# Performance work log

Measured on AMD Instinct MI355X. Metric: run time of the kernel, lower is better.

Reference implementation:

```python
import jax, jax.numpy as jnp
import numpy as np

N, C, H, W = 16, 512, 32, 32
OC = C // 8  # shrink = 8


def setup_inputs() -> dict:
    key = jax.random.key(0)
    ks = jax.random.split(key, 8)
    s = lambda fan: 1.0 / np.sqrt(fan)
    return {
        "tensor": jax.random.normal(ks[0], (N, C, H, W), dtype=jnp.float32),
        "key_w": jax.random.normal(ks[1], (OC, C), dtype=jnp.float32) * s(C),
        "key_b": jax.random.normal(ks[2], (OC,), dtype=jnp.float32) * 0.01,
        "query_w": jax.random.normal(ks[3], (OC, C), dtype=jnp.float32) * s(C),
        "query_b": jax.random.normal(ks[4], (OC,), dtype=jnp.float32) * 0.01,
        "value_w": jax.random.normal(ks[5], (C, C), dtype=jnp.float32) * s(C),
        "value_b": jax.random.normal(ks[6], (C,), dtype=jnp.float32) * 0.01,
        "gamma": jax.random.normal(ks[7], (1,), dtype=jnp.float32),
    }


def reference(tensor, key_w, key_b, query_w, query_b, value_w, value_b, gamma):
    n, c, h, w = tensor.shape
    x = tensor.reshape(n, c, h * w)  # [n, c, hw]
    # 1x1 convs are per-position linear maps over channels
    k = jnp.einsum("oc,ncp->nop", key_w, x) + key_b[None, :, None]      # [n, oc, hw]
    q = jnp.einsum("oc,ncp->nop", query_w, x) + query_b[None, :, None]  # [n, oc, hw]
    v = jnp.einsum("oc,ncp->nop", value_w, x) + value_b[None, :, None]  # [n, c, hw]
    # unscaled attention: softmax over keys (last dim)
    scores = jnp.einsum("ncq,nck->nqk", q, k)  # [n, hw, hw]
    attn = jax.nn.softmax(scores, axis=2)
    o = jnp.einsum("nck,nqk->ncq", v, attn).reshape(n, c, h, w)
    return tensor + o * gamma[0]
```

## Files before the change

kernel.cpp:

```cpp
#include <hip/hip_runtime.h>
#include <hip/hip_bf16.h>

typedef __hip_bfloat16 bf16;
typedef __attribute__((ext_vector_type(8))) short bf16x8;
typedef __attribute__((ext_vector_type(4))) float f32x4;

#define NBATCH 16
#define CCH    512
#define PP     1024
#define OCH    64

__device__ __forceinline__ void gload16(const void* g, void* l) {
  __builtin_amdgcn_global_load_lds(
      (const __attribute__((address_space(1))) void*)g,
      (__attribute__((address_space(3))) void*)l, 16, 0, 0);
}
__device__ __forceinline__ float bf2f(bf16 v) { return __bfloat162float(v); }
__device__ __forceinline__ bf16  f2bf(float v) { return __float2bfloat16(v); }

__device__ __forceinline__ void barrier_vm0() {
  asm volatile("s_waitcnt vmcnt(0)" ::: "memory");
  __builtin_amdgcn_s_barrier();
  asm volatile("" ::: "memory");
}
__device__ __forceinline__ void barrier_lgkm0() {
  asm volatile("s_waitcnt lgkmcnt(0)" ::: "memory");
  __builtin_amdgcn_s_barrier();
  asm volatile("" ::: "memory");
}

__global__ __launch_bounds__(256) void prep_transpose_kernel(
    const float* __restrict__ x,
    const float* __restrict__ key_w, const float* __restrict__ key_b,
    const float* __restrict__ query_w, const float* __restrict__ query_b,
    const float* __restrict__ value_w, const float* __restrict__ value_b,
    bf16* __restrict__ xhi, bf16* __restrict__ xlo,
    bf16* __restrict__ wqk_hi, bf16* __restrict__ wqk_lo,
    bf16* __restrict__ wv, float* __restrict__ bias_qk, float* __restrict__ bias_v) {
  __shared__ float tile[64 * 65];
  const int bid = blockIdx.x;
  const int tid = threadIdx.x;
  if (bid < 2048) {
    const int pt = bid & 15, ct = (bid >> 4) & 7, n = bid >> 7;
    const size_t xbase = ((size_t)n * CCH + ct * 64) * PP + pt * 64;
#pragma unroll
    for (int i = 0; i < 4; ++i) {
      const int chunk = i * 256 + tid;
      const int row = chunk >> 4, c4 = chunk & 15;
      const f32x4 v = *(const f32x4*)&x[xbase + (size_t)row * PP + c4 * 4];
#pragma unroll
      for (int m = 0; m < 4; ++m) tile[row * 65 + c4 * 4 + m] = v[m];
    }
    __syncthreads();
    const size_t obase = ((size_t)n * PP + pt * 64) * CCH + ct * 64;
#pragma unroll
    for (int ii = 0; ii < 2; ++ii) {
      const int p = ii * 32 + (tid >> 3);
      const int cu = tid & 7;
      bf16x8 hv, lv;
#pragma unroll
      for (int j = 0; j < 8; ++j) {
        const float f = tile[(cu * 8 + j) * 65 + p];
        const bf16 h = f2bf(f);
        const bf16 lo_ = f2bf(f - bf2f(h));
        short hs, ls;
        __builtin_memcpy(&hs, &h, 2);
        __builtin_memcpy(&ls, &lo_, 2);
        hv[j] = hs;
        lv[j] = ls;
      }
      const size_t oidx = obase + (size_t)p * CCH + cu * 8;
      *(bf16x8*)&xhi[oidx] = hv;
      *(bf16x8*)&xlo[oidx] = lv;
    }
  } else {
    const int t = (bid - 2048) * 256 + tid;
    const int TOT_QK = 128 * 512;
    const int TOT_V  = 512 * 512;
    if (t < TOT_QK) {
      const int m = t >> 9, c = t & 511;
      const float v = (m < 64) ? query_w[m * 512 + c] : key_w[(m - 64) * 512 + c];
      const bf16 hi = f2bf(v);
      wqk_hi[t] = hi;
      wqk_lo[t] = f2bf(v - bf2f(hi));
    } else if (t < TOT_QK + TOT_V) {
      const int u = t - TOT_QK;
      wv[u] = f2bf(value_w[u]);
    } else if (t < TOT_QK + TOT_V + 128) {
      const int m = t - (TOT_QK + TOT_V);
      bias_qk[m] = (m < 64) ? query_b[m] : key_b[m - 64];
    } else if (t < TOT_QK + TOT_V + 128 + 512) {
      const int m = t - (TOT_QK + TOT_V + 128);
      bias_v[m] = value_b[m];
    }
  }
}

__global__ __launch_bounds__(256) void gemm_qkv_kernel(
    const bf16* __restrict__ Whi, const bf16* __restrict__ Wlo,
    const bf16* __restrict__ Wv,
    const bf16* __restrict__ XThi, const bf16* __restrict__ XTlo,
    const float* __restrict__ biasqk, const float* __restrict__ biasv,
    bf16* __restrict__ qhi, bf16* __restrict__ qlo,
    bf16* __restrict__ khi, bf16* __restrict__ klo,
    bf16* __restrict__ Vout) {
  __shared__ __align__(16) bf16 sm[4 * 128 * 64];
  const int tid = threadIdx.x, l = tid & 63, w = tid >> 6;
  const int lrow = l >> 3, lcol = (l & 7) * 8, wr = w >> 1, wc = w & 1;
  const f32x4 z = {0.f, 0.f, 0.f, 0.f};
  f32x4 acc[4][4];
#pragma unroll
  for (int i = 0; i < 4; ++i)
#pragma unroll
    for (int j = 0; j < 4; ++j) acc[i][j] = z;

  if (blockIdx.x < 128) {
    const int id = blockIdx.x;
    const int n0 = (id & 7) * 128, bn = id >> 3;
    const size_t xoff = (size_t)bn * PP * CCH;
    bf16* Ash = sm;
    bf16* Asl = sm + 8192;
    bf16* Bsh = sm + 16384;
    bf16* Bsl = sm + 24576;
    for (int kt = 0; kt < CCH; kt += 64) {
#pragma unroll
      for (int it = 0; it < 4; ++it) {
        const int chunk = w * 4 + it;
        const int ar = chunk * 8 + lrow;
        const int br = n0 + chunk * 8 + lrow;
        gload16(Whi + (size_t)ar * CCH + kt + lcol, &Ash[chunk * 512]);
        gload16(Wlo + (size_t)ar * CCH + kt + lcol, &Asl[chunk * 512]);
        gload16(XThi + xoff + (size_t)br * CCH + kt + lcol, &Bsh[chunk * 512]);
        gload16(XTlo + xoff + (size_t)br * CCH + kt + lcol, &Bsl[chunk * 512]);
      }
      __syncthreads();
#pragma unroll
      for (int kk = 0; kk < 2; ++kk) {
        bf16x8 ah[4], al[4], bh[4], bl[4];
        const int ko = kk * 32 + (l >> 4) * 8;
#pragma unroll
        for (int i = 0; i < 4; ++i) {
          const int r = (wr * 64 + i * 16 + (l & 15)) * 64 + ko;
          ah[i] = *(const bf16x8*)&Ash[r];
          al[i] = *(const bf16x8*)&Asl[r];
        }
#pragma unroll
        for (int j = 0; j < 4; ++j) {
          const int r = (wc * 64 + j * 16 + (l & 15)) * 64 + ko;
          bh[j] = *(const bf16x8*)&Bsh[r];
          bl[j] = *(const bf16x8*)&Bsl[r];
        }
#pragma unroll
        for (int i = 0; i < 4; ++i)
#pragma unroll
          for (int j = 0; j < 4; ++j) {
            acc[i][j] = __builtin_amdgcn_mfma_f32_16x16x32_bf16(ah[i], bh[j], acc[i][j], 0, 0, 0);
            acc[i][j] = __builtin_amdgcn_mfma_f32_16x16x32_bf16(ah[i], bl[j], acc[i][j], 0, 0, 0);
            acc[i][j] = __builtin_amdgcn_mfma_f32_16x16x32_bf16(al[i], bh[j], acc[i][j], 0, 0, 0);
          }
      }
      __syncthreads();
    }
    const size_t qoff = (size_t)bn * PP * OCH;
#pragma unroll
    for (int i = 0; i < 4; ++i)
#pragma unroll
      for (int j = 0; j < 4; ++j)
#pragma unroll
        for (int r = 0; r < 4; ++r) {
          const int m = wr * 64 + i * 16 + (l >> 4) * 4 + r;
          const int p = n0 + wc * 64 + j * 16 + (l & 15);
          const float v = acc[i][j][r] + biasqk[m];
          const bf16 hi = f2bf(v);
          const bf16 lo = f2bf(v - bf2f(hi));
          if (m < 64) {
            qhi[qoff + (size_t)p * OCH + m] = hi;
            qlo[qoff + (size_t)p * OCH + m] = lo;
          } else {
            khi[qoff + (size_t)p * OCH + (m - 64)] = hi;
            klo[qoff + (size_t)p * OCH + (m - 64)] = lo;
          }
        }
  } else {
    const int id = blockIdx.x - 128;
    const int n0 = (id & 7) * 128, m0 = ((id >> 3) & 3) * 128, bn = id >> 5;
    const size_t xoff = (size_t)bn * PP * CCH;
    bf16* As = sm;
    bf16* Bs = sm + 8192;
    for (int kt = 0; kt < CCH; kt += 64) {
#pragma unroll
      for (int it = 0; it < 4; ++it) {
        const int chunk = w * 4 + it;
        gload16(Wv + (size_t)(m0 + chunk * 8 + lrow) * CCH + kt + lcol, &As[chunk * 512]);
        gload16(XThi + xoff + (size_t)(n0 + chunk * 8 + lrow) * CCH + kt + lcol, &Bs[chunk * 512]);
      }
      __syncthreads();
#pragma unroll
      for (int kk = 0; kk < 2; ++kk) {
        bf16x8 a[4], b[4];
        const int ko = kk * 32 + (l >> 4) * 8;
#pragma unroll
        for (int i = 0; i < 4; ++i) a[i] = *(const bf16x8*)&As[(wr * 64 + i * 16 + (l & 15)) * 64 + ko];
#pragma unroll
        for (int j = 0; j < 4; ++j) b[j] = *(const bf16x8*)&Bs[(wc * 64 + j * 16 + (l & 15)) * 64 + ko];
#pragma unroll
        for (int i = 0; i < 4; ++i)
#pragma unroll
          for (int j = 0; j < 4; ++j)
            acc[i][j] = __builtin_amdgcn_mfma_f32_16x16x32_bf16(a[i], b[j], acc[i][j], 0, 0, 0);
      }
      __syncthreads();
    }
#pragma unroll
    for (int i = 0; i < 4; ++i)
#pragma unroll
      for (int j = 0; j < 4; ++j)
#pragma unroll
        for (int r = 0; r < 4; ++r) {
          const int m = m0 + wr * 64 + i * 16 + (l >> 4) * 4 + r;
          const int p = n0 + wc * 64 + j * 16 + (l & 15);
          Vout[(size_t)bn * CCH * PP + (size_t)m * PP + p] = f2bf(acc[i][j][r] + biasv[m]);
        }
  }
}

#define KT 32
#define NT 32

__global__ __launch_bounds__(512, 2) void fused_attn_kernel(
    const bf16* __restrict__ qhi, const bf16* __restrict__ qlo,
    const bf16* __restrict__ khi, const bf16* __restrict__ klo,
    const bf16* __restrict__ vbuf, const float* __restrict__ tensor,
    const float* __restrict__ gamma, float* __restrict__ out) {
  __shared__ __align__(16) char smem[102400];
  __shared__ float red[128];
  __shared__ float fq[64];
  const int tid = threadIdx.x, l = tid & 63, w = tid >> 6;

  const int d = blockIdx.x;
  const int idx = d >> 3;
  const int bn = (d & 7) * 2 + (idx >> 4);
  const int qt0 = (idx & 15) * 64;

  const size_t qkoff = (size_t)bn * PP * OCH;
  const size_t voff  = (size_t)bn * CCH * PP;
  char* Qh = smem;
  char* Ql = smem + 8192;
  char* Pb = smem + 98304;

  {
    const int s = (w << 6) | l;
    const int row = s >> 3, pu = s & 7, lu = pu ^ (row & 7);
    const size_t src = qkoff + (size_t)(qt0 + row) * OCH + lu * 8;
    gload16(qhi + src, Qh + w * 1024);
    gload16(qlo + src, Ql + w * 1024);
  }
  barrier_vm0();

  bf16x8 ah[2], al[2];
  {
    const int qrow = ((w & 3) << 4) + (l & 15);
#pragma unroll
    for (int h = 0; h < 2; ++h) {
      const int lu = (l >> 4) + 4 * h, pu = lu ^ (qrow & 7);
      ah[h] = *(const bf16x8*)(Qh + qrow * 128 + pu * 16);
      al[h] = *(const bf16x8*)(Ql + qrow * 128 + pu * 16);
    }
  }

  auto stage_kv = [&](int t, char* khD, char* klD, char* vD) {
    {
      const int s = ((w & 3) << 6) | l;
      const int row = s >> 3, pu = s & 7, lu = pu ^ (row & 7);
      const bf16* srcp = ((w < 4) ? khi : klo) + qkoff + (size_t)(t * KT + row) * OCH + lu * 8;
      gload16(srcp, ((w < 4) ? khD : klD) + (w & 3) * 1024);
    }
#pragma unroll
    for (int c4 = 0; c4 < 4; ++c4) {
      const int s = (w << 8) + (c4 << 6) + l;
      const int row = s >> 2, pu = s & 3, lu = pu ^ ((row >> 1) & 3);
      const bf16* srcp = vbuf + voff + (size_t)row * PP + t * KT + lu * 8;
      gload16(srcp, vD + ((w << 8) + (c4 << 6)) * 16);
    }
  };

  stage_kv(0, smem + 16384, smem + 24576, smem + 32768);

  f32x4 acc[4][4];
  const f32x4 z = {0.f, 0.f, 0.f, 0.f};
#pragma unroll
  for (int i = 0; i < 4; ++i)
#pragma unroll
    for (int j = 0; j < 4; ++j) acc[i][j] = z;
  float psum[4] = {0.f, 0.f, 0.f, 0.f};
  const int kf = w >> 2;

  for (int t = 0; t < NT; ++t) {
    char* khB = smem + 16384 + ((t & 1) ? 4096 : 0);
    char* klB = smem + 24576 + ((t & 1) ? 4096 : 0);
    char* vB  = smem + 32768 + ((t & 1) ? 32768 : 0);

    barrier_vm0();

    if (t + 1 < NT) {
      stage_kv(t + 1,
               smem + 16384 + ((t & 1) ? 0 : 4096),
               smem + 24576 + ((t & 1) ? 0 : 4096),
               smem + 32768 + ((t & 1) ? 0 : 32768));
    }

    bf16x8 kh_[2], kl_[2];
    const int krow = (kf << 4) + (l & 15);
#pragma unroll
    for (int h = 0; h < 2; ++h) {
      const int lu = (l >> 4) + 4 * h, pu = lu ^ (krow & 7);
      kh_[h] = *(const bf16x8*)(khB + krow * 128 + pu * 16);
      kl_[h] = *(const bf16x8*)(klB + krow * 128 + pu * 16);
    }
    __builtin_amdgcn_s_setprio(1);
    f32x4 s = z;
    s = __builtin_amdgcn_mfma_f32_16x16x32_bf16(ah[0], kh_[0], s, 0, 0, 0);
    s = __builtin_amdgcn_mfma_f32_16x16x32_bf16(ah[1], kh_[1], s, 0, 0, 0);
    s = __builtin_amdgcn_mfma_f32_16x16x32_bf16(al[0], kh_[0], s, 0, 0, 0);
    s = __builtin_amdgcn_mfma_f32_16x16x32_bf16(al[1], kh_[1], s, 0, 0, 0);
    s = __builtin_amdgcn_mfma_f32_16x16x32_bf16(ah[0], kl_[0], s, 0, 0, 0);
    s = __builtin_amdgcn_mfma_f32_16x16x32_bf16(ah[1], kl_[1], s, 0, 0, 0);
    __builtin_amdgcn_s_setprio(0);

#pragma unroll
    for (int r = 0; r < 4; ++r) {
      const float pv = __expf(s[r] - 30.f);
      const bf16 pb16 = f2bf(pv);
      psum[r] += bf2f(pb16);
      const int q = ((w & 3) << 4) + ((l >> 4) << 2) + r;
      const int k = (kf << 4) + (l & 15);
      const int pu = (k >> 3) ^ ((q >> 1) & 3);
      *(bf16*)(Pb + q * 64 + pu * 16 + (k & 7) * 2) = pb16;
    }
    barrier_lgkm0();

    bf16x8 va[4], pb[4];
#pragma unroll
    for (int i = 0; i < 4; ++i) {
      const int crow = (w << 6) + (i << 4) + (l & 15);
      const int pu = (l >> 4) ^ ((crow >> 1) & 3);
      va[i] = *(const bf16x8*)(vB + crow * 64 + pu * 16);
    }
#pragma unroll
    for (int j = 0; j < 4; ++j) {
      const int prow = (j << 4) + (l & 15);
      const int pu = (l >> 4) ^ ((prow >> 1) & 3);
      pb[j] = *(const bf16x8*)(Pb + prow * 64 + pu * 16);
    }
    __builtin_amdgcn_s_setprio(1);
#pragma unroll
    for (int i = 0; i < 4; ++i)
#pragma unroll
      for (int j = 0; j < 4; ++j)
        acc[i][j] = __builtin_amdgcn_mfma_f32_16x16x32_bf16(va[i], pb[j], acc[i][j], 0, 0, 0);
    __builtin_amdgcn_s_setprio(0);
  }

  f32x4 tv0[8];
#pragma unroll
  for (int it = 0; it < 8; ++it) {
    const int chunk = it * 512 + tid;
    const int cl = chunk >> 4, ch = chunk & 15;
    tv0[it] = *(const f32x4*)&tensor[((size_t)bn * CCH + cl) * PP + qt0 + ch * 4];
  }

#pragma unroll
  for (int off = 1; off < 16; off <<= 1)
#pragma unroll
    for (int r = 0; r < 4; ++r) psum[r] += __shfl_xor(psum[r], off);
  if ((l & 15) == 0) {
#pragma unroll
    for (int r = 0; r < 4; ++r) {
      const int q = ((w & 3) << 4) + ((l >> 4) << 2) + r;
      red[q * 2 + kf] = psum[r];
    }
  }
  __syncthreads();
  if (tid < 64) fq[tid] = gamma[0] / (red[tid * 2] + red[tid * 2 + 1]);
  __syncthreads();

  float* rep = (float*)smem;
  for (int half = 0; half < 2; ++half) {
    if ((w >> 2) == half) {
#pragma unroll
      for (int i = 0; i < 4; ++i)
#pragma unroll
        for (int j = 0; j < 4; ++j) {
          const int q = (j << 4) + (l & 15);
          const float f = fq[q];
          const int c0 = ((w & 3) << 6) + (i << 4) + ((l >> 4) << 2);
#pragma unroll
          for (int r = 0; r < 4; ++r) rep[(c0 + r) * 68 + q] = acc[i][j][r] * f;
        }
    }
    __syncthreads();
#pragma unroll
    for (int it = 0; it < 8; ++it) {
      const int chunk = it * 512 + tid;
      const int cl = chunk >> 4, ch = chunk & 15;
      const size_t gi = ((size_t)bn * CCH + half * 256 + cl) * PP + qt0 + ch * 4;
      const f32x4 tv = (half == 0) ? tv0[it] : *(const f32x4*)&tensor[gi];
      const f32x4 rv = *(const f32x4*)&rep[cl * 68 + ch * 4];
      *(f32x4*)&out[gi] = tv + rv;
    }
    __syncthreads();
  }
}

extern "C" void kernel_launch(void* const* d_in, const int* in_sizes, int n_in,
                              void* d_out, int out_size, void* d_ws, size_t ws_size,
                              hipStream_t stream) {
  const float* tensor  = (const float*)d_in[0];
  const float* key_w   = (const float*)d_in[1];
  const float* key_b   = (const float*)d_in[2];
  const float* query_w = (const float*)d_in[3];
  const float* query_b = (const float*)d_in[4];
  const float* value_w = (const float*)d_in[5];
  const float* value_b = (const float*)d_in[6];
  const float* gamma   = (const float*)d_in[7];

  char* ws = (char*)d_ws;
  size_t off = 0;
  auto alloc = [&](size_t bytes) -> char* {
    char* p = ws + off;
    off += (bytes + 255) & ~(size_t)255;
    return p;
  };
  bf16* xt_hi  = (bf16*)alloc((size_t)NBATCH * PP * CCH * 2);
  bf16* xt_lo  = (bf16*)alloc((size_t)NBATCH * PP * CCH * 2);
  bf16* wqk_hi = (bf16*)alloc(128 * 512 * 2);
  bf16* wqk_lo = (bf16*)alloc(128 * 512 * 2);
  bf16* wv     = (bf16*)alloc(512 * 512 * 2);
  float* bias_qk = (float*)alloc(128 * 4);
  float* bias_v  = (float*)alloc(512 * 4);
  bf16* q_hi = (bf16*)alloc((size_t)NBATCH * PP * OCH * 2);
  bf16* q_lo = (bf16*)alloc((size_t)NBATCH * PP * OCH * 2);
  bf16* k_hi = (bf16*)alloc((size_t)NBATCH * PP * OCH * 2);
  bf16* k_lo = (bf16*)alloc((size_t)NBATCH * PP * OCH * 2);
  bf16* vbuf = (bf16*)alloc((size_t)NBATCH * CCH * PP * 2);
  (void)ws_size; (void)in_sizes; (void)n_in; (void)out_size;

  prep_transpose_kernel<<<dim3(3331), dim3(256), 0, stream>>>(
      tensor, key_w, key_b, query_w, query_b, value_w, value_b,
      xt_hi, xt_lo, wqk_hi, wqk_lo, wv, bias_qk, bias_v);

  gemm_qkv_kernel<<<dim3(640), dim3(256), 0, stream>>>(
      wqk_hi, wqk_lo, wv, xt_hi, xt_lo, bias_qk, bias_v,
      q_hi, q_lo, k_hi, k_lo, vbuf);

  fused_attn_kernel<<<dim3(256), dim3(512), 0, stream>>>(
      q_hi, q_lo, k_hi, k_lo, vbuf, tensor, gamma, (float*)d_out);
}
```

Measured before the change: 96.39 us.

## Fuse input transpose and bf16 split into QKV GEMM tile loading

Removes the separate pass that transposed the fp32 input into hi/lo bf16 copies in workspace. The QKV GEMM now loads fp32 input tiles straight into shared memory, then converts and transposes them in LDS into an XOR-swizzled layout before the MFMA loop. This drops a full write and re-read of two large bf16 intermediates. In exchange, each GEMM block repeats the conversion work, and the 640 blocks re-read the fp32 input redundantly (4 V blocks plus 1 QK block per tile). It also adds extra barriers per k-step.

```diff
diff --git a/kernel.cpp b/kernel.cpp
--- a/kernel.cpp
+++ b/kernel.cpp
@@ -29,126 +29,123 @@
   asm volatile("" ::: "memory");
 }
 
-__global__ __launch_bounds__(256) void prep_transpose_kernel(
-    const float* __restrict__ x,
-    const float* __restrict__ key_w, const float* __restrict__ key_b,
-    const float* __restrict__ query_w, const float* __restrict__ query_b,
-    const float* __restrict__ value_w, const float* __restrict__ value_b,
-    bf16* __restrict__ xhi, bf16* __restrict__ xlo,
-    bf16* __restrict__ wqk_hi, bf16* __restrict__ wqk_lo,
-    bf16* __restrict__ wv, float* __restrict__ bias_qk, float* __restrict__ bias_v) {
-  __shared__ float tile[64 * 65];
-  const int bid = blockIdx.x;
-  const int tid = threadIdx.x;
-  if (bid < 2048) {
-    const int pt = bid & 15, ct = (bid >> 4) & 7, n = bid >> 7;
-    const size_t xbase = ((size_t)n * CCH + ct * 64) * PP + pt * 64;
-#pragma unroll
-    for (int i = 0; i < 4; ++i) {
-      const int chunk = i * 256 + tid;
-      const int row = chunk >> 4, c4 = chunk & 15;
-      const f32x4 v = *(const f32x4*)&x[xbase + (size_t)row * PP + c4 * 4];
-#pragma unroll
-      for (int m = 0; m < 4; ++m) tile[row * 65 + c4 * 4 + m] = v[m];
-    }
-    __syncthreads();
-    const size_t obase = ((size_t)n * PP + pt * 64) * CCH + ct * 64;
-#pragma unroll
-    for (int ii = 0; ii < 2; ++ii) {
-      const int p = ii * 32 + (tid >> 3);
-      const int cu = tid & 7;
-      bf16x8 hv, lv;
-#pragma unroll
-      for (int j = 0; j < 8; ++j) {
-        const float f = tile[(cu * 8 + j) * 65 + p];
-        const bf16 h = f2bf(f);
-        const bf16 lo_ = f2bf(f - bf2f(h));
-        short hs, ls;
-        __builtin_memcpy(&hs, &h, 2);
-        __builtin_memcpy(&ls, &lo_, 2);
-        hv[j] = hs;
-        lv[j] = ls;
-      }
-      const size_t oidx = obase + (size_t)p * CCH + cu * 8;
-      *(bf16x8*)&xhi[oidx] = hv;
-      *(bf16x8*)&xlo[oidx] = lv;
-    }
-  } else {
-    const int t = (bid - 2048) * 256 + tid;
-    const int TOT_QK = 128 * 512;
-    const int TOT_V  = 512 * 512;
-    if (t < TOT_QK) {
-      const int m = t >> 9, c = t & 511;
-      const float v = (m < 64) ? query_w[m * 512 + c] : key_w[(m - 64) * 512 + c];
-      const bf16 hi = f2bf(v);
-      wqk_hi[t] = hi;
-      wqk_lo[t] = f2bf(v - bf2f(hi));
-    } else if (t < TOT_QK + TOT_V) {
-      const int u = t - TOT_QK;
-      wv[u] = f2bf(value_w[u]);
-    } else if (t < TOT_QK + TOT_V + 128) {
-      const int m = t - (TOT_QK + TOT_V);
-      bias_qk[m] = (m < 64) ? query_b[m] : key_b[m - 64];
-    } else if (t < TOT_QK + TOT_V + 128 + 512) {
-      const int m = t - (TOT_QK + TOT_V + 128);
-      bias_v[m] = value_b[m];
-    }
+__global__ void prep_kernel(const float* __restrict__ key_w, const float* __restrict__ key_b,
+                            const float* __restrict__ query_w, const float* __restrict__ query_b,
+                            const float* __restrict__ value_w, const float* __restrict__ value_b,
+                            bf16* __restrict__ wqk_hi, bf16* __restrict__ wqk_lo,
+                            bf16* __restrict__ wv, float* __restrict__ bias_qk,
+                            float* __restrict__ bias_v) {
+  const int t = blockIdx.x * blockDim.x + threadIdx.x;
+  const int TOT_QK = 128 * 512;
+  const int TOT_V  = 512 * 512;
+  if (t < TOT_QK) {
+    const int m = t >> 9, c = t & 511;
+    const float v = (m < 64) ? query_w[m * 512 + c] : key_w[(m - 64) * 512 + c];
+    const bf16 hi = f2bf(v);
+    wqk_hi[t] = hi;
+    wqk_lo[t] = f2bf(v - bf2f(hi));
+  } else if (t < TOT_QK + TOT_V) {
+    const int u = t - TOT_QK;
+    wv[u] = f2bf(value_w[u]);
+  } else if (t < TOT_QK + TOT_V + 128) {
+    const int m = t - (TOT_QK + TOT_V);
+    bias_qk[m] = (m < 64) ? query_b[m] : key_b[m - 64];
+  } else if (t < TOT_QK + TOT_V + 128 + 512) {
+    const int m = t - (TOT_QK + TOT_V + 128);
+    bias_v[m] = value_b[m];
   }
 }
 
 __global__ __launch_bounds__(256) void gemm_qkv_kernel(
     const bf16* __restrict__ Whi, const bf16* __restrict__ Wlo,
-    const bf16* __restrict__ Wv,
-    const bf16* __restrict__ XThi, const bf16* __restrict__ XTlo,
+    const bf16* __restrict__ Wv, const float* __restrict__ x,
     const float* __restrict__ biasqk, const float* __restrict__ biasv,
     bf16* __restrict__ qhi, bf16* __restrict__ qlo,
     bf16* __restrict__ khi, bf16* __restrict__ klo,
     bf16* __restrict__ Vout) {
-  __shared__ __align__(16) bf16 sm[4 * 128 * 64];
+  __shared__ __align__(16) char sm[65536];
   const int tid = threadIdx.x, l = tid & 63, w = tid >> 6;
+  const int li = l & 15, g = l >> 4;
   const int lrow = l >> 3, lcol = (l & 7) * 8, wr = w >> 1, wc = w & 1;
+  const int tp = tid >> 1;
+  const int tch = (tid & 1) * 32;
   const f32x4 z = {0.f, 0.f, 0.f, 0.f};
   f32x4 acc[4][4];
 #pragma unroll
   for (int i = 0; i < 4; ++i)
 #pragma unroll
     for (int j = 0; j < 4; ++j) acc[i][j] = z;
+
+  char* Xs  = sm + 32768;
+  char* Bsh = sm + 32768;
+  char* Bsl = sm + 49152;
 
   if (blockIdx.x < 128) {
     const int id = blockIdx.x;
     const int n0 = (id & 7) * 128, bn = id >> 3;
-    const size_t xoff = (size_t)bn * PP * CCH;
-    bf16* Ash = sm;
-    bf16* Asl = sm + 8192;
-    bf16* Bsh = sm + 16384;
-    bf16* Bsl = sm + 24576;
+    const float* xb = x + (size_t)bn * CCH * PP;
+    bf16* Ash = (bf16*)sm;
+    bf16* Asl = (bf16*)(sm + 16384);
+
     for (int kt = 0; kt < CCH; kt += 64) {
 #pragma unroll
       for (int it = 0; it < 4; ++it) {
         const int chunk = w * 4 + it;
         const int ar = chunk * 8 + lrow;
-        const int br = n0 + chunk * 8 + lrow;
         gload16(Whi + (size_t)ar * CCH + kt + lcol, &Ash[chunk * 512]);
         gload16(Wlo + (size_t)ar * CCH + kt + lcol, &Asl[chunk * 512]);
-        gload16(XThi + xoff + (size_t)br * CCH + kt + lcol, &Bsh[chunk * 512]);
-        gload16(XTlo + xoff + (size_t)br * CCH + kt + lcol, &Bsl[chunk * 512]);
+      }
+#pragma unroll
+      for (int i = 0; i < 8; ++i) {
+        const int s = i * 256 + w * 64 + l;
+        const int row = s >> 5, col16 = s & 31;
+        gload16(xb + (size_t)(kt + row) * PP + n0 + col16 * 4,
+                Xs + (i * 256 + w * 64) * 16);
       }
       __syncthreads();
+
+      float f[32];
+#pragma unroll
+      for (int k = 0; k < 32; ++k)
+        f[k] = *(const float*)(Xs + (size_t)(tch + k) * 512 + tp * 4);
+      barrier_lgkm0();
+#pragma unroll
+      for (int k2 = 0; k2 < 4; ++k2) {
+        bf16x8 hv, lv;
+#pragma unroll
+        for (int j = 0; j < 8; ++j) {
+          const float ff = f[k2 * 8 + j];
+          const bf16 h = f2bf(ff);
+          const bf16 lo_ = f2bf(ff - bf2f(h));
+          short hs, ls;
+          __builtin_memcpy(&hs, &h, 2);
+          __builtin_memcpy(&ls, &lo_, 2);
+          hv[j] = hs;
+          lv[j] = ls;
+        }
+        const int chunk = (tch >> 3) + k2;
+        const int pu = chunk ^ (tp & 7);
+        *(bf16x8*)(Bsh + tp * 128 + pu * 16) = hv;
+        *(bf16x8*)(Bsl + tp * 128 + pu * 16) = lv;
+      }
+      barrier_lgkm0();
+
 #pragma unroll
       for (int kk = 0; kk < 2; ++kk) {
         bf16x8 ah[4], al[4], bh[4], bl[4];
-        const int ko = kk * 32 + (l >> 4) * 8;
+        const int ko = kk * 32 + g * 8;
 #pragma unroll
         for (int i = 0; i < 4; ++i) {
-          const int r = (wr * 64 + i * 16 + (l & 15)) * 64 + ko;
+          const int r = (wr * 64 + i * 16 + li) * 64 + ko;
           ah[i] = *(const bf16x8*)&Ash[r];
           al[i] = *(const bf16x8*)&Asl[r];
         }
 #pragma unroll
         for (int j = 0; j < 4; ++j) {
-          const int r = (wc * 64 + j * 16 + (l & 15)) * 64 + ko;
-          bh[j] = *(const bf16x8*)&Bsh[r];
-          bl[j] = *(const bf16x8*)&Bsl[r];
+          const int row = wc * 64 + j * 16 + li;
+          const int pu = (4 * kk + g) ^ (row & 7);
+          bh[j] = *(const bf16x8*)(Bsh + row * 128 + pu * 16);
+          bl[j] = *(const bf16x8*)(Bsl + row * 128 + pu * 16);
         }
 #pragma unroll
         for (int i = 0; i < 4; ++i)
@@ -168,8 +165,8 @@
       for (int j = 0; j < 4; ++j)
 #pragma unroll
         for (int r = 0; r < 4; ++r) {
-          const int m = wr * 64 + i * 16 + (l >> 4) * 4 + r;
-          const int p = n0 + wc * 64 + j * 16 + (l & 15);
+          const int m = wr * 64 + i * 16 + g * 4 + r;
+          const int p = n0 + wc * 64 + j * 16 + li;
           const float v = acc[i][j][r] + biasqk[m];
           const bf16 hi = f2bf(v);
           const bf16 lo = f2bf(v - bf2f(hi));
@@ -184,25 +181,57 @@
   } else {
     const int id = blockIdx.x - 128;
     const int n0 = (id & 7) * 128, m0 = ((id >> 3) & 3) * 128, bn = id >> 5;
-    const size_t xoff = (size_t)bn * PP * CCH;
-    bf16* As = sm;
-    bf16* Bs = sm + 8192;
+    const float* xb = x + (size_t)bn * CCH * PP;
+    bf16* As = (bf16*)sm;
+
     for (int kt = 0; kt < CCH; kt += 64) {
 #pragma unroll
       for (int it = 0; it < 4; ++it) {
         const int chunk = w * 4 + it;
         gload16(Wv + (size_t)(m0 + chunk * 8 + lrow) * CCH + kt + lcol, &As[chunk * 512]);
-        gload16(XThi + xoff + (size_t)(n0 + chunk * 8 + lrow) * CCH + kt + lcol, &Bs[chunk * 512]);
+      }
+#pragma unroll
+      for (int i = 0; i < 8; ++i) {
+        const int s = i * 256 + w * 64 + l;
+        const int row = s >> 5, col16 = s & 31;
+        gload16(xb + (size_t)(kt + row) * PP + n0 + col16 * 4,
+                Xs + (i * 256 + w * 64) * 16);
       }
       __syncthreads();
+
+      float f[32];
+#pragma unroll
+      for (int k = 0; k < 32; ++k)
+        f[k] = *(const float*)(Xs + (size_t)(tch + k) * 512 + tp * 4);
+      barrier_lgkm0();
+#pragma unroll
+      for (int k2 = 0; k2 < 4; ++k2) {
+        bf16x8 hv;
+#pragma unroll
+        for (int j = 0; j < 8; ++j) {
+          const bf16 h = f2bf(f[k2 * 8 + j]);
+          short hs;
+          __builtin_memcpy(&hs, &h, 2);
+          hv[j] = hs;
+        }
+        const int chunk = (tch >> 3) + k2;
+        const int pu = chunk ^ (tp & 7);
+        *(bf16x8*)(Bsh + tp * 128 + pu * 16) = hv;
+      }
+      barrier_lgkm0();
+
 #pragma unroll
       for (int kk = 0; kk < 2; ++kk) {
         bf16x8 a[4], b[4];
-        const int ko = kk * 32 + (l >> 4) * 8;
-#pragma unroll
-        for (int i = 0; i < 4; ++i) a[i] = *(const bf16x8*)&As[(wr * 64 + i * 16 + (l & 15)) * 64 + ko];
-#pragma unroll
-        for (int j = 0; j < 4; ++j) b[j] = *(const bf16x8*)&Bs[(wc * 64 + j * 16 + (l & 15)) * 64 + ko];
+        const int ko = kk * 32 + g * 8;
+#pragma unroll
+        for (int i = 0; i < 4; ++i) a[i] = *(const bf16x8*)&As[(wr * 64 + i * 16 + li) * 64 + ko];
+#pragma unroll
+        for (int j = 0; j < 4; ++j) {
+          const int row = wc * 64 + j * 16 + li;
+          const int pu = (4 * kk + g) ^ (row & 7);
+          b[j] = *(const bf16x8*)(Bsh + row * 128 + pu * 16);
+        }
 #pragma unroll
         for (int i = 0; i < 4; ++i)
 #pragma unroll
@@ -217,8 +246,8 @@
       for (int j = 0; j < 4; ++j)
 #pragma unroll
         for (int r = 0; r < 4; ++r) {
-          const int m = m0 + wr * 64 + i * 16 + (l >> 4) * 4 + r;
-          const int p = n0 + wc * 64 + j * 16 + (l & 15);
+          const int m = m0 + wr * 64 + i * 16 + g * 4 + r;
+          const int p = n0 + wc * 64 + j * 16 + li;
           Vout[(size_t)bn * CCH * PP + (size_t)m * PP + p] = f2bf(acc[i][j][r] + biasv[m]);
         }
   }
@@ -431,8 +460,6 @@
     off += (bytes + 255) & ~(size_t)255;
     return p;
   };
-  bf16* xt_hi  = (bf16*)alloc((size_t)NBATCH * PP * CCH * 2);
-  bf16* xt_lo  = (bf16*)alloc((size_t)NBATCH * PP * CCH * 2);
   bf16* wqk_hi = (bf16*)alloc(128 * 512 * 2);
   bf16* wqk_lo = (bf16*)alloc(128 * 512 * 2);
   bf16* wv     = (bf16*)alloc(512 * 512 * 2);
@@ -445,12 +472,12 @@
   bf16* vbuf = (bf16*)alloc((size_t)NBATCH * CCH * PP * 2);
   (void)ws_size; (void)in_sizes; (void)n_in; (void)out_size;
 
-  prep_transpose_kernel<<<dim3(3331), dim3(256), 0, stream>>>(
-      tensor, key_w, key_b, query_w, query_b, value_w, value_b,
-      xt_hi, xt_lo, wqk_hi, wqk_lo, wv, bias_qk, bias_v);
+  prep_kernel<<<dim3(1283), dim3(256), 0, stream>>>(
+      key_w, key_b, query_w, query_b, value_w, value_b,
+      wqk_hi, wqk_lo, wv, bias_qk, bias_v);
 
   gemm_qkv_kernel<<<dim3(640), dim3(256), 0, stream>>>(
-      wqk_hi, wqk_lo, wv, xt_hi, xt_lo, bias_qk, bias_v,
+      wqk_hi, wqk_lo, wv, tensor, bias_qk, bias_v,
       q_hi, q_lo, k_hi, k_lo, vbuf);
 
   fused_attn_kernel<<<dim3(256), dim3(512), 0, stream>>>(
```

Result: faster. 91.70 us (-4.9%).
